# Kernel tuning notes

Measured on AMD Instinct MI355X. Metric: run time of the kernel, lower is better.

Reference implementation:

```python
import jax, jax.numpy as jnp
import numpy as np
from jax import lax

N_BLOCKS = 5
POOL = 15
N_HEADS = 8
LATENT = 32
N_EXPERTS = 4


def setup_inputs() -> dict:
    key = jax.random.key(0)
    ks = jax.random.split(key, 24)
    B, T, D = 4, 2048, 512
    H = 2 * D  # expert_dim
    s = 0.02
    f = lambda k, shp: (jax.random.normal(k, shp, jnp.float32) * s)
    return {
        'x': jax.random.normal(ks[0], (B, T, D), jnp.float32),
        # TemporalGating gate_proj
        'tg_w': f(ks[1], (D, N_BLOCKS)), 'tg_b': jnp.zeros((N_BLOCKS,), jnp.float32),
        # DualScaleFusion
        'mp_w': f(ks[2], (D, D)), 'mp_b': jnp.zeros((D,), jnp.float32),
        'fu_w': f(ks[3], (2 * D, D)), 'fu_b': jnp.zeros((D,), jnp.float32),
        # MLAAttention (all no-bias)
        'wc': f(ks[4], (D, LATENT)), 'wk': f(ks[5], (LATENT, D)),
        'wv': f(ks[6], (LATENT, D)), 'wq': f(ks[7], (D, D)), 'wo': f(ks[8], (D, D)),
        # RMSNorms
        's1': jnp.ones((D,), jnp.float32), 's2': jnp.ones((D,), jnp.float32),
        # GatedMoE
        'wr': f(ks[9], (D, N_EXPERTS)), 'br': jnp.zeros((N_EXPERTS,), jnp.float32),
        'wg': f(ks[10], (D, D)), 'bg': jnp.zeros((D,), jnp.float32),
        'w1': f(ks[11], (N_EXPERTS, D, H)), 'b1': jnp.zeros((N_EXPERTS, H), jnp.float32),
        'w2': f(ks[12], (N_EXPERTS, H, D)), 'b2': jnp.zeros((N_EXPERTS, D), jnp.float32),
    }


def _temporal_gate(x, tg_w, tg_b):
    B, T, D = x.shape
    bs = T // N_BLOCKS
    tl = N_BLOCKS * bs
    r = x[:, :tl].reshape(B, N_BLOCKS, bs, D)          # [B,nb,bs,D]
    bm = r.mean(axis=2)                                 # [B,nb,D]
    imp = jax.nn.softmax(bm @ tg_w + tg_b, axis=-1)     # [B,nb,nb]
    imp = imp.mean(axis=-1, keepdims=True)              # [B,nb,1]
    g = (r * imp[..., None]).reshape(B, tl, D)
    return jnp.pad(g, ((0, 0), (0, T - tl), (0, 0)))


def _dual_scale(x, mp_w, mp_b, fu_w, fu_b):
    # AveragePooling1D(pool=15, stride=1, SAME): TF excludes padding from the mean.
    B, T, D = x.shape
    sums = lax.reduce_window(x, 0.0, lax.add, (1, POOL, 1), (1, 1, 1), 'SAME')
    cnt = lax.reduce_window(jnp.ones((1, T, 1), x.dtype), 0.0, lax.add,
                            (1, POOL, 1), (1, 1, 1), 'SAME')
    macro = sums / cnt
    macro_feat = macro @ mp_w + mp_b
    return jnp.concatenate([x, macro_feat], axis=-1) @ fu_w + fu_b


def _mla_attn(x, wc, wk, wv, wq, wo):
    B, T, D = x.shape
    dh = D // N_HEADS
    split = lambda t: t.reshape(B, T, N_HEADS, dh).transpose(0, 2, 1, 3)
    latent = x @ wc                                      # [B,T,L]
    K, V, Q = split(latent @ wk), split(latent @ wv), split(x @ wq)
    scores = jnp.einsum('bhqd,bhkd->bhqk', Q, K) / jnp.sqrt(jnp.float32(dh))
    causal = jnp.tril(jnp.ones((T, T), jnp.float32))
    scores = scores + (1.0 - causal) * -1e9
    attn = jax.nn.softmax(scores, axis=-1)
    out = jnp.einsum('bhqk,bhkd->bhqd', attn, V).transpose(0, 2, 1, 3).reshape(B, T, D)
    return out @ wo


def _rmsnorm(x, scale, eps=1e-6):
    var = jnp.mean(jnp.square(x), axis=-1, keepdims=True)
    return scale * (x * lax.rsqrt(var + eps))


def _moe(x, wr, br, wg, bg, w1, b1, w2, b2):
    w = jax.nn.softmax(x @ wr + br, axis=-1)             # [B,T,E]
    xg = x * jax.nn.sigmoid(x @ wg + bg)
    h = jax.nn.gelu(jnp.einsum('btd,edh->bteh', xg, w1) + b1, approximate=False)
    eo = jnp.einsum('bteh,ehd->bted', h, w2) + b2        # [B,T,E,D]
    return jnp.einsum('bted,bte->btd', eo, w)


def reference(x, tg_w, tg_b, mp_w, mp_b, fu_w, fu_b, wc, wk, wv, wq, wo,
              s1, s2, wr, br, wg, bg, w1, b1, w2, b2):
    xf = _temporal_gate(x, tg_w, tg_b)
    xfu = _dual_scale(xf, mp_w, mp_b, fu_w, fu_b)
    x1 = _rmsnorm(x + _mla_attn(xfu, wc, wk, wv, wq, wo), s1)
    return _rmsnorm(x1 + _moe(x1, wr, br, wg, bg, w1, b1, w2, b2), s2)
```

## Files before the change

### kernel.cpp

```cpp
#include <hip/hip_runtime.h>
#include <math.h>

#define B_   4
#define T_   2048
#define D_   512
#define TOK  (B_*T_)
#define TL_  2045
#define GATE 0.2f
#define QSCALE 0.18033688011112043f

typedef unsigned short u16;
typedef __attribute__((ext_vector_type(8))) short short8;
typedef __attribute__((ext_vector_type(4))) float f32x4;

static __device__ __forceinline__ u16 f2u(float f){
    union { float f; unsigned u; } a; a.f = f;
    unsigned r = a.u + 0x7fffu + ((a.u >> 16) & 1u);
    return (u16)(r >> 16);
}
static __device__ __forceinline__ float u2f(u16 u){
    union { unsigned u; float f; } a; a.u = ((unsigned)u) << 16;
    return a.f;
}
static __device__ __forceinline__ f32x4 mfma16(short8 a, short8 b, f32x4 c){
    return __builtin_amdgcn_mfma_f32_16x16x32_bf16(a, b, c, 0, 0, 0);
}
static __device__ __forceinline__ void glds16(const u16* g, u16* l){
    __builtin_amdgcn_global_load_lds((const __attribute__((address_space(1))) void*)g,
                                     (__attribute__((address_space(3))) void*)l, 16, 0, 0);
}

__global__ __launch_bounds__(256) void gatepool_kernel(
    const float* __restrict__ x, u16* __restrict__ xfcat)
{
    int idx = blockIdx.x*256 + threadIdx.x;
    int d = idx & 511, g = idx >> 9;
    int b = g >> 7, t0 = (g & 127) << 4;
    const float* xp = x + ((size_t)b*2048)*512 + d;
    float v[30];
    #pragma unroll
    for (int j = 0; j < 30; ++j){
        int u = t0 - 7 + j;
        v[j] = (u >= 0 && u < TL_) ? xp[(size_t)u*512] : 0.f;
    }
    float p[31]; p[0] = 0.f;
    #pragma unroll
    for (int j = 0; j < 30; ++j) p[j+1] = p[j] + v[j];
    u16* xc = xfcat + ((size_t)(b*2048 + t0))*1024 + d;
    #pragma unroll
    for (int i = 0; i < 16; ++i){
        int t = t0 + i;
        float sum = p[i+15] - p[i];
        int lo = t-7; if (lo < 0) lo = 0;
        int hi = t+7; if (hi > 2047) hi = 2047;
        xc[(size_t)i*1024]       = f2u((t < TL_) ? GATE*v[i+7] : 0.f);
        xc[(size_t)i*1024 + 512] = f2u(GATE * sum / (float)(hi - lo + 1));
    }
}

struct TJob { const float* src; u16* dst; int K, N, ldout, coloff, tiles; float scale; };
struct TJobs { TJob j[13]; int n; };

__global__ __launch_bounds__(256) void tconv_all_kernel(TJobs JJ){
    __shared__ float t[32][33];
    int idx = blockIdx.x;
    int jb = 0;
    while (jb < JJ.n - 1 && idx >= JJ.j[jb].tiles){ idx -= JJ.j[jb].tiles; ++jb; }
    TJob J = JJ.j[jb];
    int tX = J.N >> 5;
    int k0 = (idx / tX) * 32, n0 = (idx % tX) * 32;
    int tx = threadIdx.x & 31, ty = threadIdx.x >> 5;
    #pragma unroll
    for (int i = 0; i < 32; i += 8)
        t[ty+i][tx] = J.src[(size_t)(k0+ty+i)*J.N + n0+tx];
    __syncthreads();
    #pragma unroll
    for (int i = 0; i < 32; i += 8)
        J.dst[(size_t)(n0+ty+i)*J.ldout + J.coloff + k0+tx] = f2u(J.scale * t[tx][ty+i]);
}

__global__ void convert_kernel(const float* __restrict__ in, u16* __restrict__ out){
    int idx = blockIdx.x*256 + threadIdx.x;
    out[idx] = f2u(in[idx]);
}

__global__ __launch_bounds__(256) void biasfold_kernel(
    const float* __restrict__ fu_b, const float* __restrict__ mp_b,
    const float* __restrict__ fu_w, float* __restrict__ out)
{
    int n = blockIdx.x, tid = threadIdx.x;
    float s = mp_b[tid]*fu_w[(size_t)(512+tid)*512 + n]
            + mp_b[tid+256]*fu_w[(size_t)(768+tid)*512 + n];
    for (int off = 32; off; off >>= 1) s += __shfl_down(s, off);
    __shared__ float ws[4];
    if ((tid & 63) == 0) ws[tid >> 6] = s;
    __syncthreads();
    if (tid == 0) out[n] = fu_b[n] + ws[0]+ws[1]+ws[2]+ws[3];
}

__global__ __launch_bounds__(256) void qkvbias_kernel(
    const float* __restrict__ fubias, const u16* __restrict__ wqkvT,
    float* __restrict__ out)
{
    int n = blockIdx.x, tid = threadIdx.x;
    const u16* wp = wqkvT + (size_t)n*512;
    float s = fubias[tid]*u2f(wp[tid]) + fubias[tid+256]*u2f(wp[tid+256]);
    for (int off = 32; off; off >>= 1) s += __shfl_down(s, off);
    __shared__ float ws[4];
    if ((tid & 63) == 0) ws[tid >> 6] = s;
    __syncthreads();
    if (tid == 0) out[n] = ws[0]+ws[1]+ws[2]+ws[3];
}

__global__ __launch_bounds__(256) void sgemm_kernel(const float* __restrict__ A,
    const float* __restrict__ B, u16* __restrict__ dstT, int K){
    __shared__ float As[16][65];
    __shared__ float Bs[16][65];
    int tid = threadIdx.x;
    int tx = tid & 15, ty = tid >> 4;
    int m0 = blockIdx.y*64, n0 = blockIdx.x*64;
    int arow = tid >> 2, akq = (tid & 3) * 4;
    int bk = tid >> 4, bn = (tid & 15) * 4;
    float acc[4][4] = {};
    for (int k0 = 0; k0 < K; k0 += 16){
        const float* Ap = A + (size_t)(m0+arow)*K + k0 + akq;
        As[akq+0][arow]=Ap[0]; As[akq+1][arow]=Ap[1];
        As[akq+2][arow]=Ap[2]; As[akq+3][arow]=Ap[3];
        const float* Bp = B + (size_t)(k0+bk)*512 + n0 + bn;
        Bs[bk][bn+0]=Bp[0]; Bs[bk][bn+1]=Bp[1];
        Bs[bk][bn+2]=Bp[2]; Bs[bk][bn+3]=Bp[3];
        __syncthreads();
        #pragma unroll
        for (int kk = 0; kk < 16; ++kk){
            float av[4], bv[4];
            #pragma unroll
            for (int i=0;i<4;++i) av[i]=As[kk][ty*4+i];
            #pragma unroll
            for (int j=0;j<4;++j) bv[j]=Bs[kk][tx*4+j];
            #pragma unroll
            for (int i=0;i<4;++i)
                #pragma unroll
                for (int j=0;j<4;++j) acc[i][j] += av[i]*bv[j];
        }
        __syncthreads();
    }
    #pragma unroll
    for (int i=0;i<4;++i)
        #pragma unroll
        for (int j=0;j<4;++j)
            dstT[(size_t)(n0+tx*4+j)*512 + m0+ty*4+i] = f2u(acc[i][j]);
}

#define GF_GELU   1
#define GF_RSCOL  4
#define GF_GLU    8
#define GF_QKV    32

template<int MT>
__global__ __launch_bounds__(256) void mgemm_kernel(
    const u16* __restrict__ A, int lda, const u16* __restrict__ Bt, int ldb,
    const float* __restrict__ bias, const float* __restrict__ rs,
    const u16* __restrict__ glu, void* __restrict__ Cp, int ldc,
    u16* __restrict__ Cp2, int K, int flags)
{
    constexpr int MI = MT/32;
    __shared__ u16 As[MT*64];
    __shared__ u16 Bs[128*64];
    int tid = threadIdx.x;
    int wave = tid >> 6, lane = tid & 63;
    int n16 = lane & 15, quad = lane >> 4;
    int m0 = blockIdx.y * MT, n0 = blockIdx.x * 128;
    int wr = (wave >> 1) * (MT/2), wc = (wave & 1) * 64;

    f32x4 acc[MI][4] = {};

    for (int k0 = 0; k0 < K; k0 += 64){
        #pragma unroll
        for (int i = 0; i < MT/32; ++i){
            int s = i*256 + tid;
            int row = s >> 3, g = (s & 7) ^ (row & 7);
            glds16(A + (size_t)(m0+row)*lda + k0 + g*8, As + (size_t)s*8);
        }
        #pragma unroll
        for (int i = 0; i < 4; ++i){
            int s = i*256 + tid;
            int row = s >> 3, g = (s & 7) ^ (row & 7);
            glds16(Bt + (size_t)(n0+row)*ldb + k0 + g*8, Bs + (size_t)s*8);
        }
        __syncthreads();
        #pragma unroll
        for (int ks = 0; ks < 2; ++ks){
            short8 af[MI], bf[4];
            #pragma unroll
            for (int mi = 0; mi < MI; ++mi){
                int row = wr + mi*16 + n16;
                int g = (ks*4 + quad) ^ (row & 7);
                af[mi] = *(const short8*)&As[row*64 + g*8];
            }
            #pragma unroll
            for (int ni = 0; ni < 4; ++ni){
                int row = wc + ni*16 + n16;
                int g = (ks*4 + quad) ^ (row & 7);
                bf[ni] = *(const short8*)&Bs[row*64 + g*8];
            }
            #pragma unroll
            for (int mi = 0; mi < MI; ++mi)
                #pragma unroll
                for (int ni = 0; ni < 4; ++ni)
                    acc[mi][ni] = mfma16(af[mi], bf[ni], acc[mi][ni]);
        }
        __syncthreads();
    }

    if ((flags & GF_QKV) && n0 >= 1024){
        #pragma unroll
        for (int mi = 0; mi < MI; ++mi){
            int row0 = m0 + wr + mi*16 + quad*4;
            #pragma unroll
            for (int ni = 0; ni < 4; ++ni){
                int col = n0 + wc + ni*16 + n16;
                float bb = bias[col];
                ushort4 h4;
                h4.x = f2u(acc[mi][ni][0] + bb); h4.y = f2u(acc[mi][ni][1] + bb);
                h4.z = f2u(acc[mi][ni][2] + bb); h4.w = f2u(acc[mi][ni][3] + bb);
                *(ushort4*)&Cp2[(size_t)(col-1024)*8192 + row0] = h4;
            }
        }
        return;
    }

    #pragma unroll
    for (int mi = 0; mi < MI; ++mi){
        #pragma unroll
        for (int reg = 0; reg < 4; ++reg){
            int row = m0 + wr + mi*16 + quad*4 + reg;
            #pragma unroll
            for (int ni = 0; ni < 4; ++ni){
                int col = n0 + wc + ni*16 + n16;
                float v = acc[mi][ni][reg];
                if (bias) v += bias[col];
                if (flags & GF_GELU)  v = 0.5f*v*(1.f + erff(v*0.70710678118f));
                if (flags & GF_GLU)   v = u2f(glu[(size_t)row*512 + col]) / (1.f + __expf(-v));
                if (flags & GF_RSCOL) v *= rs[(size_t)row*4 + (col >> 10)];
                ((u16*)Cp)[(size_t)row*ldc + col] = f2u(v);
            }
        }
    }
}

__global__ __launch_bounds__(256) void flash_kernel(
    const u16* __restrict__ QK,
    const u16* __restrict__ VT,
    u16* __restrict__ O)
{
    int bid = blockIdx.x;
    int qt = 15 - (bid >> 5);
    int bh = bid & 31;
    int h = bh & 7, b = bh >> 3;
    __shared__ u16 Ks[64*64];
    __shared__ u16 Vt[64*64];
    __shared__ u16 Ps[4][32*64];
    int tid = threadIdx.x;
    int wave = tid >> 6, lane = tid & 63;
    int n16 = lane & 15, quad = lane >> 4;
    size_t btok = (size_t)b*2048;
    size_t tok0 = btok + qt*128;

    short8 qf[2][2];
    #pragma unroll
    for (int g = 0; g < 2; ++g)
        #pragma unroll
        for (int ks = 0; ks < 2; ++ks)
            qf[g][ks] = *(const short8*)&QK[(tok0 + wave*32 + g*16 + n16)*1024
                                           + h*64 + ks*32 + quad*8];

    int qlo[2];  qlo[0] = qt*128 + wave*32; qlo[1] = qlo[0] + 16;
    int qrow[2]; qrow[0] = qlo[0] + n16;    qrow[1] = qlo[1] + n16;
    float m_st[2] = {-3.0e38f, -3.0e38f}, l_st[2] = {0.f, 0.f};
    f32x4 ov[2][4] = {};

    int nkt = 2*qt + 2;
    for (int kt = 0; kt < nkt; ++kt){
        __syncthreads();
        {
            int r = tid >> 2;
            int g0 = (tid & 3) * 2;
            const uint4* kp = (const uint4*)&QK[(btok + kt*64 + r)*1024 + 512 + h*64 + g0*8];
            uint4 ka = kp[0], kb = kp[1];
            *(uint4*)&Ks[r*64 + ((g0  ) ^ (r&7))*8] = ka;
            *(uint4*)&Ks[r*64 + ((g0+1) ^ (r&7))*8] = kb;
            const uint4* vp = (const uint4*)&VT[(size_t)(h*64 + r)*8192 + btok + kt*64 + g0*8];
            uint4 va = vp[0], vb = vp[1];
            *(uint4*)&Vt[r*64 + ((g0  ) ^ (r&7))*8] = va;
            *(uint4*)&Vt[r*64 + ((g0+1) ^ (r&7))*8] = vb;
        }
        __syncthreads();

        bool act[2];
        #pragma unroll
        for (int g = 0; g < 2; ++g){
            act[g] = (kt*64 <= qlo[g] + 15);
            if (!act[g]) continue;
            f32x4 st[4];
            #pragma unroll
            for (int ct = 0; ct < 4; ++ct){
                f32x4 a = {};
                #pragma unroll
                for (int ks = 0; ks < 2; ++ks){
                    short8 kf = *(const short8*)&Ks[(ct*16+n16)*64 + (((ks*4+quad) ^ (n16&7))*8)];
                    a = mfma16(kf, qf[g][ks], a);
                }
                st[ct] = a;
            }
            if (kt*64 + 63 > qlo[g]){
                #pragma unroll
                for (int ct = 0; ct < 4; ++ct){
                    int kb0 = kt*64 + ct*16 + quad*4;
                    #pragma unroll
                    for (int r = 0; r < 4; ++r)
                        if (kb0 + r > qrow[g]) st[ct][r] = -3.0e38f;
                }
            }
            float mx = fmaxf(fmaxf(fmaxf(st[0][0],st[0][1]),fmaxf(st[0][2],st[0][3])),
                       fmaxf(fmaxf(fmaxf(st[1][0],st[1][1]),fmaxf(st[1][2],st[1][3])),
                       fmaxf(fmaxf(fmaxf(st[2][0],st[2][1]),fmaxf(st[2][2],st[2][3])),
                             fmaxf(fmaxf(st[3][0],st[3][1]),fmaxf(st[3][2],st[3][3])))));
            mx = fmaxf(mx, __shfl_xor(mx, 16));
            mx = fmaxf(mx, __shfl_xor(mx, 32));
            float mn = fmaxf(m_st[g], mx);
            float al = exp2f(m_st[g] - mn);
            m_st[g] = mn;
            float sum = 0.f;
            #pragma unroll
            for (int ct = 0; ct < 4; ++ct)
                #pragma unroll
                for (int r = 0; r < 4; ++r){
                    float p = exp2f(st[ct][r] - mn);
                    st[ct][r] = p; sum += p;
                }
            sum += __shfl_xor(sum, 16);
            sum += __shfl_xor(sum, 32);
            l_st[g] = l_st[g]*al + sum;
            int qr = g*16 + n16;
            #pragma unroll
            for (int ct = 0; ct < 4; ++ct){
                ushort4 h4;
                h4.x = f2u(st[ct][0]); h4.y = f2u(st[ct][1]);
                h4.z = f2u(st[ct][2]); h4.w = f2u(st[ct][3]);
                int goff = ct*2 + (quad >> 1);
                *(ushort4*)&Ps[wave][qr*64 + ((goff ^ (qr&7))*8) + (quad&1)*4] = h4;
            }
            #pragma unroll
            for (int r = 0; r < 4; ++r){
                float aa = __shfl(al, quad*4 + r);
                #pragma unroll
                for (int dt = 0; dt < 4; ++dt) ov[g][dt][r] *= aa;
            }
        }
        #pragma unroll
        for (int g = 0; g < 2; ++g){
            if (!act[g]) continue;
            short8 ap[2];
            int row = g*16 + n16;
            #pragma unroll
            for (int ks = 0; ks < 2; ++ks)
                ap[ks] = *(const short8*)&Ps[wave][row*64 + (((ks*4+quad) ^ (row&7))*8)];
            #pragma unroll
            for (int dt = 0; dt < 4; ++dt)
                #pragma unroll
                for (int ks = 0; ks < 2; ++ks){
                    short8 bv = *(const short8*)&Vt[(dt*16+n16)*64 + (((ks*4+quad) ^ (n16&7))*8)];
                    ov[g][dt] = mfma16(ap[ks], bv, ov[g][dt]);
                }
        }
    }
    #pragma unroll
    for (int g = 0; g < 2; ++g)
        #pragma unroll
        for (int r = 0; r < 4; ++r){
            float li = __shfl(l_st[g], quad*4 + r);
            float inv = 1.f / li;
            size_t row = tok0 + wave*32 + g*16 + quad*4 + r;
            #pragma unroll
            for (int dt = 0; dt < 4; ++dt)
                O[row*512 + h*64 + dt*16 + n16] = f2u(ov[g][dt][r] * inv);
        }
}

__global__ __launch_bounds__(256) void rmsnorm_kernel(
    const float* __restrict__ x, const u16* __restrict__ y,
    const float* __restrict__ scale, u16* __restrict__ out)
{
    int tok = blockIdx.x, tid = threadIdx.x;
    size_t base = (size_t)tok * 512;
    float v0 = x[base+tid]     + u2f(y[base+tid]);
    float v1 = x[base+tid+256] + u2f(y[base+tid+256]);
    float ss = v0*v0 + v1*v1;
    for (int off = 32; off; off >>= 1) ss += __shfl_down(ss, off);
    __shared__ float ws[4];
    if ((tid & 63) == 0) ws[tid >> 6] = ss;
    __syncthreads();
    float rstd = rsqrtf((ws[0]+ws[1]+ws[2]+ws[3])*(1.f/512.f) + 1e-6f);
    out[base+tid]     = f2u(scale[tid]     * v0 * rstd);
    out[base+tid+256] = f2u(scale[tid+256] * v1 * rstd);
}

__global__ __launch_bounds__(256) void final_kernel(
    const u16* __restrict__ x1, const u16* __restrict__ moe,
    const float* __restrict__ rout, const float* __restrict__ b2,
    const float* __restrict__ scale, float* __restrict__ out)
{
    int tok = blockIdx.x, tid = threadIdx.x;
    size_t base = (size_t)tok * 512;
    float r0 = rout[tok*4+0], r1 = rout[tok*4+1], r2 = rout[tok*4+2], r3 = rout[tok*4+3];
    float bb0 = r0*b2[tid]     + r1*b2[512+tid]     + r2*b2[1024+tid]     + r3*b2[1536+tid];
    float bb1 = r0*b2[tid+256] + r1*b2[768+tid]     + r2*b2[1280+tid]     + r3*b2[1792+tid];
    float v0 = u2f(x1[base+tid])     + u2f(moe[base+tid])     + bb0;
    float v1 = u2f(x1[base+tid+256]) + u2f(moe[base+tid+256]) + bb1;
    float ss = v0*v0 + v1*v1;
    for (int off = 32; off; off >>= 1) ss += __shfl_down(ss, off);
    __shared__ float ws[4];
    if ((tid & 63) == 0) ws[tid >> 6] = ss;
    __syncthreads();
    float rstd = rsqrtf((ws[0]+ws[1]+ws[2]+ws[3])*(1.f/512.f) + 1e-6f);
    out[base+tid]     = scale[tid]     * v0 * rstd;
    out[base+tid+256] = scale[tid+256] * v1 * rstd;
}

__global__ __launch_bounds__(256) void router_kernel(
    const u16* __restrict__ x1, const float* __restrict__ wr,
    const float* __restrict__ br, float* __restrict__ rout)
{
    int wid = threadIdx.x >> 6, lane = threadIdx.x & 63;
    int tok = blockIdx.x*4 + wid;
    const u16* xp = x1 + (size_t)tok*512;
    float p0=0.f, p1=0.f, p2=0.f, p3=0.f;
    for (int d = lane; d < 512; d += 64){
        float xv = u2f(xp[d]);
        p0 += xv*wr[d*4+0]; p1 += xv*wr[d*4+1];
        p2 += xv*wr[d*4+2]; p3 += xv*wr[d*4+3];
    }
    for (int off = 32; off; off >>= 1){
        p0 += __shfl_down(p0,off); p1 += __shfl_down(p1,off);
        p2 += __shfl_down(p2,off); p3 += __shfl_down(p3,off);
    }
    if (lane == 0){
        p0 += br[0]; p1 += br[1]; p2 += br[2]; p3 += br[3];
        float mx = fmaxf(fmaxf(p0,p1), fmaxf(p2,p3));
        float e0=__expf(p0-mx), e1=__expf(p1-mx), e2=__expf(p2-mx), e3=__expf(p3-mx);
        float inv = 1.f/(e0+e1+e2+e3);
        rout[tok*4+0]=e0*inv; rout[tok*4+1]=e1*inv;
        rout[tok*4+2]=e2*inv; rout[tok*4+3]=e3*inv;
    }
}

extern "C" void kernel_launch(void* const* d_in, const int* in_sizes, int n_in,
                              void* d_out, int out_size, void* d_ws, size_t ws_size,
                              hipStream_t stream)
{
    const float* x    = (const float*)d_in[0];
    const float* mp_w = (const float*)d_in[3];
    const float* mp_b = (const float*)d_in[4];
    const float* fu_w = (const float*)d_in[5];
    const float* fu_b = (const float*)d_in[6];
    const float* wc   = (const float*)d_in[7];
    const float* wk   = (const float*)d_in[8];
    const float* wv   = (const float*)d_in[9];
    const float* wq   = (const float*)d_in[10];
    const float* wo   = (const float*)d_in[11];
    const float* s1   = (const float*)d_in[12];
    const float* s2   = (const float*)d_in[13];
    const float* wr   = (const float*)d_in[14];
    const float* br   = (const float*)d_in[15];
    const float* wg   = (const float*)d_in[16];
    const float* bg   = (const float*)d_in[17];
    const float* w1   = (const float*)d_in[18];
    const float* b1   = (const float*)d_in[19];
    const float* w2   = (const float*)d_in[20];
    const float* b2   = (const float*)d_in[21];

    char* wsb = (char*)d_ws;
    const size_t MB = 1024*1024;
    u16*   WqkvC  = (u16*)(wsb + 0);
    u16*   woT    = (u16*)(wsb + 3*MB);
    u16*   wgT    = (u16*)(wsb + 3*MB + 512*1024);
    u16*   w1T    = (u16*)(wsb + 4*MB);
    u16*   w2Ts   = (u16*)(wsb + 8*MB);
    float* fubias = (float*)(wsb + 12*MB);
    float* qkvbias= (float*)(wsb + 12*MB + 4096);
    float* ROUT   = (float*)(wsb + 12*MB + 16384);
    u16*   wqkvT  = (u16*)(wsb + 25*MB/2);
    u16*   fuBT   = (u16*)(wsb + 14*MB);
    u16*   mp_wB  = (u16*)(wsb + 29*MB/2);
    u16*   WfuBF  = (u16*)(wsb + 15*MB);
    u16*   XFcat = (u16*)(wsb + 16*MB);
    u16*   S3    = (u16*)(wsb + 16*MB);
    u16*   MOE   = (u16*)(wsb + 16*MB);
    u16*   x1h   = (u16*)(wsb + 24*MB);
    u16*   QKb   = (u16*)(wsb + 32*MB);
    u16*   XG    = (u16*)(wsb + 32*MB);
    u16*   Hb    = (u16*)(wsb + 40*MB);
    u16*   VbT   = (u16*)(wsb + 48*MB);
    u16*   ATT   = (u16*)(wsb + 56*MB);

    auto mg128 = [&](const u16* A, int lda, const u16* Bt, int ldb, const float* bias,
                     const float* rs, const u16* glu, void* C, int ldc, u16* C2,
                     int M, int N, int K, int flags){
        dim3 g(N/128, M/128);
        mgemm_kernel<128><<<g, 256, 0, stream>>>(A, lda, Bt, ldb, bias, rs, glu, C, ldc, C2, K, flags);
    };
    auto mg64 = [&](const u16* A, int lda, const u16* Bt, int ldb, const float* bias,
                    const float* rs, const u16* glu, void* C, int ldc, u16* C2,
                    int M, int N, int K, int flags){
        dim3 g(N/128, M/64);
        mgemm_kernel<64><<<g, 256, 0, stream>>>(A, lda, Bt, ldb, bias, rs, glu, C, ldc, C2, K, flags);
    };

    TJobs JJ; JJ.n = 11;
    auto setj = [&](int i, const float* src, u16* dst, int K, int N, int ldout,
                    int coloff, float scale){
        JJ.j[i] = TJob{src, dst, K, N, ldout, coloff, (K/32)*(N/32), scale};
    };
    setj(0, wq,            wqkvT, 512,  512,  512, 0, QSCALE);
    setj(1, wo,            woT,   512,  512,  512, 0, 1.f);
    setj(2, wg,            wgT,   512,  512,  512, 0, 1.f);
    setj(3, fu_w + 512*512,fuBT,  512,  512,  512, 0, 1.f);
    for (int e = 0; e < 4; ++e){
        setj(4+e, w1 + (size_t)e*512*1024, w1T + (size_t)e*1024*512, 512, 1024, 512, 0, 1.f);
        setj(8+e, w2 + (size_t)e*1024*512, w2Ts + (size_t)e*1024, 1024, 512, 4096, 0, 1.f);
    }
    int nt = 4*256 + 8*512;
    tconv_all_kernel<<<nt, 256, 0, stream>>>(JJ);
    convert_kernel<<<512*512/256, 256, 0, stream>>>(mp_w, mp_wB);
    convert_kernel<<<512*512/256, 256, 0, stream>>>(fu_w, WfuBF);
    sgemm_kernel<<<dim3(8,8), 256, 0, stream>>>(wc, wk, wqkvT + 512*512, 32);
    sgemm_kernel<<<dim3(8,8), 256, 0, stream>>>(wc, wv, wqkvT + 1024*512, 32);
    biasfold_kernel<<<512, 256, 0, stream>>>(fu_b, mp_b, fu_w, fubias);
    qkvbias_kernel<<<1536, 256, 0, stream>>>(fubias, wqkvT, qkvbias);
    mg64(mp_wB, 512, fuBT, 512, 0, 0, 0, WfuBF + 512*512, 512, 0, 512, 512, 512, 0);
    mg64(wqkvT, 512, WfuBF, 512, 0, 0, 0, WqkvC, 1024, 0, 1536, 1024, 512, 0);

    gatepool_kernel<<<(TOK/16)*512/256, 256, 0, stream>>>(x, XFcat);
    mg64 (XFcat, 1024, WqkvC, 1024, qkvbias, 0, 0, QKb, 1024, VbT, TOK, 1536, 1024, GF_QKV);
    flash_kernel<<<512, 256, 0, stream>>>(QKb, VbT, ATT);
    mg64 (ATT, 512, woT, 512, 0, 0, 0, S3, 512, 0, TOK, 512, 512, 0);
    rmsnorm_kernel<<<TOK, 256, 0, stream>>>(x, S3, s1, x1h);
    router_kernel<<<TOK/4, 256, 0, stream>>>(x1h, wr, br, ROUT);
    mg64 (x1h, 512, wgT, 512, bg, 0, x1h, XG, 512, 0, TOK, 512, 512, GF_GLU);
    for (int h = 0; h < 2; ++h){
        mg128(XG + (size_t)h*4096*512, 512, w1T, 512, b1, ROUT + (size_t)h*4096*4, 0,
              Hb, 4096, 0, 4096, 4096, 512, GF_GELU | GF_RSCOL);
        mg64 (Hb, 4096, w2Ts, 4096, 0, 0, 0,
              MOE + (size_t)h*4096*512, 512, 0, 4096, 512, 4096, 0);
    }
    final_kernel<<<TOK, 256, 0, stream>>>(x1h, MOE, ROUT, b2, s2, (float*)d_out);
}
```

Baseline: 612.9 us.

## Rebalance causal flash tiles and fuse MoE halves into full-M GEMM launches

The flash kernel now uses 64-row query tiles and has each block process a mirrored pair of tiles (31-p and p), so every block does the same amount of causal work. The probability tile is converted to bf16 by truncation instead of rounding. The GEMM kernel gains a second A/C base pointer split at row 4096, which lets the QKV (now 128-row tiles), output, gate and MoE GEMMs run as single full-token launches instead of per-half loops. The MoE down-projection writes fp32 output, with an accumulate fallback path when the workspace is small. The trade-offs are less K/V reuse per loaded tile in attention, slightly less accurate probabilities, and more fp32 traffic for the MoE output.

```diff
diff --git a/kernel.cpp b/kernel.cpp
--- a/kernel.cpp
+++ b/kernel.cpp
@@ -8,6 +8,7 @@
 #define TL_  2045
 #define GATE 0.2f
 #define QSCALE 0.18033688011112043f
+#define MSPLIT 4096
 
 typedef unsigned short u16;
 typedef __attribute__((ext_vector_type(8))) short short8;
@@ -17,6 +18,9 @@
     union { float f; unsigned u; } a; a.f = f;
     unsigned r = a.u + 0x7fffu + ((a.u >> 16) & 1u);
     return (u16)(r >> 16);
+}
+static __device__ __forceinline__ u16 f2u_t(float f){
+    return (u16)(__float_as_uint(f) >> 16);
 }
 static __device__ __forceinline__ float u2f(u16 u){
     union { unsigned u; float f; } a; a.u = ((unsigned)u) << 16;
@@ -152,16 +156,19 @@
 }
 
 #define GF_GELU   1
+#define GF_ACCUM  2
 #define GF_RSCOL  4
 #define GF_GLU    8
+#define GF_F32OUT 16
 #define GF_QKV    32
 
 template<int MT>
 __global__ __launch_bounds__(256) void mgemm_kernel(
-    const u16* __restrict__ A, int lda, const u16* __restrict__ Bt, int ldb,
+    const u16* __restrict__ A, const u16* __restrict__ A2, int lda,
+    const u16* __restrict__ Bt, int ldb,
     const float* __restrict__ bias, const float* __restrict__ rs,
-    const u16* __restrict__ glu, void* __restrict__ Cp, int ldc,
-    u16* __restrict__ Cp2, int K, int flags)
+    const u16* __restrict__ glu, void* __restrict__ Cp, void* __restrict__ CpB,
+    int ldc, u16* __restrict__ Cp2, int K, int flags)
 {
     constexpr int MI = MT/32;
     __shared__ u16 As[MT*64];
@@ -179,7 +186,10 @@
         for (int i = 0; i < MT/32; ++i){
             int s = i*256 + tid;
             int row = s >> 3, g = (s & 7) ^ (row & 7);
-            glds16(A + (size_t)(m0+row)*lda + k0 + g*8, As + (size_t)s*8);
+            int rg = m0 + row;
+            const u16* Ap = (rg < MSPLIT) ? A + (size_t)rg*lda
+                                          : A2 + (size_t)(rg - MSPLIT)*lda;
+            glds16(Ap + k0 + g*8, As + (size_t)s*8);
         }
         #pragma unroll
         for (int i = 0; i < 4; ++i){
@@ -234,6 +244,8 @@
         #pragma unroll
         for (int reg = 0; reg < 4; ++reg){
             int row = m0 + wr + mi*16 + quad*4 + reg;
+            void*  cb = (row < MSPLIT) ? Cp : CpB;
+            size_t rr = (row < MSPLIT) ? row : row - MSPLIT;
             #pragma unroll
             for (int ni = 0; ni < 4; ++ni){
                 int col = n0 + wc + ni*16 + n16;
@@ -242,7 +254,10 @@
                 if (flags & GF_GELU)  v = 0.5f*v*(1.f + erff(v*0.70710678118f));
                 if (flags & GF_GLU)   v = u2f(glu[(size_t)row*512 + col]) / (1.f + __expf(-v));
                 if (flags & GF_RSCOL) v *= rs[(size_t)row*4 + (col >> 10)];
-                ((u16*)Cp)[(size_t)row*ldc + col] = f2u(v);
+                size_t ci = rr*ldc + col;
+                if (flags & GF_ACCUM)       ((float*)cb)[ci] += v;
+                else if (flags & GF_F32OUT) ((float*)cb)[ci]  = v;
+                else                        ((u16*)cb)[ci]    = f2u(v);
             }
         }
     }
@@ -254,53 +269,45 @@
     u16* __restrict__ O)
 {
     int bid = blockIdx.x;
-    int qt = 15 - (bid >> 5);
+    int p = bid >> 5;
     int bh = bid & 31;
     int h = bh & 7, b = bh >> 3;
     __shared__ u16 Ks[64*64];
     __shared__ u16 Vt[64*64];
-    __shared__ u16 Ps[4][32*64];
+    __shared__ u16 Ps[4][16*64];
     int tid = threadIdx.x;
     int wave = tid >> 6, lane = tid & 63;
     int n16 = lane & 15, quad = lane >> 4;
     size_t btok = (size_t)b*2048;
-    size_t tok0 = btok + qt*128;
-
-    short8 qf[2][2];
-    #pragma unroll
-    for (int g = 0; g < 2; ++g)
+
+    for (int ph = 0; ph < 2; ++ph){
+        int qt = ph ? p : (31 - p);
+        size_t tok0 = btok + qt*64;
+        short8 qf[2];
         #pragma unroll
         for (int ks = 0; ks < 2; ++ks)
-            qf[g][ks] = *(const short8*)&QK[(tok0 + wave*32 + g*16 + n16)*1024
-                                           + h*64 + ks*32 + quad*8];
-
-    int qlo[2];  qlo[0] = qt*128 + wave*32; qlo[1] = qlo[0] + 16;
-    int qrow[2]; qrow[0] = qlo[0] + n16;    qrow[1] = qlo[1] + n16;
-    float m_st[2] = {-3.0e38f, -3.0e38f}, l_st[2] = {0.f, 0.f};
-    f32x4 ov[2][4] = {};
-
-    int nkt = 2*qt + 2;
-    for (int kt = 0; kt < nkt; ++kt){
-        __syncthreads();
-        {
-            int r = tid >> 2;
-            int g0 = (tid & 3) * 2;
-            const uint4* kp = (const uint4*)&QK[(btok + kt*64 + r)*1024 + 512 + h*64 + g0*8];
-            uint4 ka = kp[0], kb = kp[1];
-            *(uint4*)&Ks[r*64 + ((g0  ) ^ (r&7))*8] = ka;
-            *(uint4*)&Ks[r*64 + ((g0+1) ^ (r&7))*8] = kb;
-            const uint4* vp = (const uint4*)&VT[(size_t)(h*64 + r)*8192 + btok + kt*64 + g0*8];
-            uint4 va = vp[0], vb = vp[1];
-            *(uint4*)&Vt[r*64 + ((g0  ) ^ (r&7))*8] = va;
-            *(uint4*)&Vt[r*64 + ((g0+1) ^ (r&7))*8] = vb;
-        }
-        __syncthreads();
-
-        bool act[2];
-        #pragma unroll
-        for (int g = 0; g < 2; ++g){
-            act[g] = (kt*64 <= qlo[g] + 15);
-            if (!act[g]) continue;
+            qf[ks] = *(const short8*)&QK[(tok0 + wave*16 + n16)*1024
+                                         + h*64 + ks*32 + quad*8];
+        int qrow = qt*64 + wave*16 + n16;
+        float m_st = -3.0e38f, l_st = 0.f;
+        f32x4 ov[4] = {};
+
+        for (int kt = 0; kt <= qt; ++kt){
+            __syncthreads();
+            {
+                int r = tid >> 2;
+                int g0 = (tid & 3) * 2;
+                const uint4* kp = (const uint4*)&QK[(btok + kt*64 + r)*1024 + 512 + h*64 + g0*8];
+                uint4 ka = kp[0], kb = kp[1];
+                *(uint4*)&Ks[r*64 + ((g0  ) ^ (r&7))*8] = ka;
+                *(uint4*)&Ks[r*64 + ((g0+1) ^ (r&7))*8] = kb;
+                const uint4* vp = (const uint4*)&VT[(size_t)(h*64 + r)*8192 + btok + kt*64 + g0*8];
+                uint4 va = vp[0], vb = vp[1];
+                *(uint4*)&Vt[r*64 + ((g0  ) ^ (r&7))*8] = va;
+                *(uint4*)&Vt[r*64 + ((g0+1) ^ (r&7))*8] = vb;
+            }
+            __syncthreads();
+
             f32x4 st[4];
             #pragma unroll
             for (int ct = 0; ct < 4; ++ct){
@@ -308,17 +315,17 @@
                 #pragma unroll
                 for (int ks = 0; ks < 2; ++ks){
                     short8 kf = *(const short8*)&Ks[(ct*16+n16)*64 + (((ks*4+quad) ^ (n16&7))*8)];
-                    a = mfma16(kf, qf[g][ks], a);
+                    a = mfma16(kf, qf[ks], a);
                 }
                 st[ct] = a;
             }
-            if (kt*64 + 63 > qlo[g]){
+            if (kt == qt){
                 #pragma unroll
                 for (int ct = 0; ct < 4; ++ct){
                     int kb0 = kt*64 + ct*16 + quad*4;
                     #pragma unroll
                     for (int r = 0; r < 4; ++r)
-                        if (kb0 + r > qrow[g]) st[ct][r] = -3.0e38f;
+                        if (kb0 + r > qrow) st[ct][r] = -3.0e38f;
                 }
             }
             float mx = fmaxf(fmaxf(fmaxf(st[0][0],st[0][1]),fmaxf(st[0][2],st[0][3])),
@@ -327,64 +334,56 @@
                              fmaxf(fmaxf(st[3][0],st[3][1]),fmaxf(st[3][2],st[3][3])))));
             mx = fmaxf(mx, __shfl_xor(mx, 16));
             mx = fmaxf(mx, __shfl_xor(mx, 32));
-            float mn = fmaxf(m_st[g], mx);
-            float al = exp2f(m_st[g] - mn);
-            m_st[g] = mn;
+            float mn = fmaxf(m_st, mx);
+            float al = exp2f(m_st - mn);
+            m_st = mn;
             float sum = 0.f;
             #pragma unroll
             for (int ct = 0; ct < 4; ++ct)
                 #pragma unroll
                 for (int r = 0; r < 4; ++r){
-                    float p = exp2f(st[ct][r] - mn);
-                    st[ct][r] = p; sum += p;
+                    float pp = exp2f(st[ct][r] - mn);
+                    st[ct][r] = pp; sum += pp;
                 }
             sum += __shfl_xor(sum, 16);
             sum += __shfl_xor(sum, 32);
-            l_st[g] = l_st[g]*al + sum;
-            int qr = g*16 + n16;
+            l_st = l_st*al + sum;
             #pragma unroll
             for (int ct = 0; ct < 4; ++ct){
                 ushort4 h4;
-                h4.x = f2u(st[ct][0]); h4.y = f2u(st[ct][1]);
-                h4.z = f2u(st[ct][2]); h4.w = f2u(st[ct][3]);
+                h4.x = f2u_t(st[ct][0]); h4.y = f2u_t(st[ct][1]);
+                h4.z = f2u_t(st[ct][2]); h4.w = f2u_t(st[ct][3]);
                 int goff = ct*2 + (quad >> 1);
-                *(ushort4*)&Ps[wave][qr*64 + ((goff ^ (qr&7))*8) + (quad&1)*4] = h4;
+                *(ushort4*)&Ps[wave][n16*64 + ((goff ^ (n16&7))*8) + (quad&1)*4] = h4;
             }
             #pragma unroll
             for (int r = 0; r < 4; ++r){
                 float aa = __shfl(al, quad*4 + r);
                 #pragma unroll
-                for (int dt = 0; dt < 4; ++dt) ov[g][dt][r] *= aa;
-            }
-        }
-        #pragma unroll
-        for (int g = 0; g < 2; ++g){
-            if (!act[g]) continue;
+                for (int dt = 0; dt < 4; ++dt) ov[dt][r] *= aa;
+            }
             short8 ap[2];
-            int row = g*16 + n16;
             #pragma unroll
             for (int ks = 0; ks < 2; ++ks)
-                ap[ks] = *(const short8*)&Ps[wave][row*64 + (((ks*4+quad) ^ (row&7))*8)];
+                ap[ks] = *(const short8*)&Ps[wave][n16*64 + (((ks*4+quad) ^ (n16&7))*8)];
             #pragma unroll
             for (int dt = 0; dt < 4; ++dt)
                 #pragma unroll
                 for (int ks = 0; ks < 2; ++ks){
                     short8 bv = *(const short8*)&Vt[(dt*16+n16)*64 + (((ks*4+quad) ^ (n16&7))*8)];
-                    ov[g][dt] = mfma16(ap[ks], bv, ov[g][dt]);
+                    ov[dt] = mfma16(ap[ks], bv, ov[dt]);
                 }
         }
-    }
-    #pragma unroll
-    for (int g = 0; g < 2; ++g)
         #pragma unroll
         for (int r = 0; r < 4; ++r){
-            float li = __shfl(l_st[g], quad*4 + r);
+            float li = __shfl(l_st, quad*4 + r);
             float inv = 1.f / li;
-            size_t row = tok0 + wave*32 + g*16 + quad*4 + r;
+            size_t row = tok0 + wave*16 + quad*4 + r;
             #pragma unroll
             for (int dt = 0; dt < 4; ++dt)
-                O[row*512 + h*64 + dt*16 + n16] = f2u(ov[g][dt][r] * inv);
-        }
+                O[row*512 + h*64 + dt*16 + n16] = f2u(ov[dt][r] * inv);
+        }
+    }
 }
 
 __global__ __launch_bounds__(256) void rmsnorm_kernel(
@@ -406,7 +405,7 @@
 }
 
 __global__ __launch_bounds__(256) void final_kernel(
-    const u16* __restrict__ x1, const u16* __restrict__ moe,
+    const u16* __restrict__ x1, const float* __restrict__ moe,
     const float* __restrict__ rout, const float* __restrict__ b2,
     const float* __restrict__ scale, float* __restrict__ out)
 {
@@ -415,8 +414,8 @@
     float r0 = rout[tok*4+0], r1 = rout[tok*4+1], r2 = rout[tok*4+2], r3 = rout[tok*4+3];
     float bb0 = r0*b2[tid]     + r1*b2[512+tid]     + r2*b2[1024+tid]     + r3*b2[1536+tid];
     float bb1 = r0*b2[tid+256] + r1*b2[768+tid]     + r2*b2[1280+tid]     + r3*b2[1792+tid];
-    float v0 = u2f(x1[base+tid])     + u2f(moe[base+tid])     + bb0;
-    float v1 = u2f(x1[base+tid+256]) + u2f(moe[base+tid+256]) + bb1;
+    float v0 = u2f(x1[base+tid])     + moe[base+tid]     + bb0;
+    float v1 = u2f(x1[base+tid+256]) + moe[base+tid+256] + bb1;
     float ss = v0*v0 + v1*v1;
     for (int off = 32; off; off >>= 1) ss += __shfl_down(ss, off);
     __shared__ float ws[4];
@@ -487,36 +486,40 @@
     u16*   w1T    = (u16*)(wsb + 4*MB);
     u16*   w2Ts   = (u16*)(wsb + 8*MB);
     float* fubias = (float*)(wsb + 12*MB);
-    float* qkvbias= (float*)(wsb + 12*MB + 4096);
-    float* ROUT   = (float*)(wsb + 12*MB + 16384);
-    u16*   wqkvT  = (u16*)(wsb + 25*MB/2);
-    u16*   fuBT   = (u16*)(wsb + 14*MB);
-    u16*   mp_wB  = (u16*)(wsb + 29*MB/2);
-    u16*   WfuBF  = (u16*)(wsb + 15*MB);
+    float* qkvbias= (float*)(wsb + 12*MB + 8192);
+    float* ROUT   = (float*)(wsb + 12*MB + 32768);
+    u16*   wqkvT  = (u16*)(wsb + 12*MB + 512*1024);
+    u16*   fuBT   = (u16*)(wsb + 16*MB);
+    u16*   mp_wB  = (u16*)(wsb + 16*MB + 512*1024);
+    u16*   WfuBF  = (u16*)(wsb + 17*MB);
+    u16*   x1h   = (u16*)(wsb + 14*MB);
     u16*   XFcat = (u16*)(wsb + 16*MB);
-    u16*   S3    = (u16*)(wsb + 16*MB);
-    u16*   MOE   = (u16*)(wsb + 16*MB);
-    u16*   x1h   = (u16*)(wsb + 24*MB);
+    u16*   XG    = (u16*)(wsb + 22*MB);
+    u16*   S3    = (u16*)(wsb + 24*MB);
     u16*   QKb   = (u16*)(wsb + 32*MB);
-    u16*   XG    = (u16*)(wsb + 32*MB);
-    u16*   Hb    = (u16*)(wsb + 40*MB);
+    float* MOE   = (float*)(wsb + 32*MB);
     u16*   VbT   = (u16*)(wsb + 48*MB);
     u16*   ATT   = (u16*)(wsb + 56*MB);
-
-    auto mg128 = [&](const u16* A, int lda, const u16* Bt, int ldb, const float* bias,
-                     const float* rs, const u16* glu, void* C, int ldc, u16* C2,
-                     int M, int N, int K, int flags){
+    u16*   HbA   = (u16*)(wsb + 48*MB);
+    u16*   HbB   = (u16*)(wsb + 80*MB);
+    bool big = ws_size >= (size_t)112*MB;
+
+    auto mg128 = [&](const u16* A, const u16* A2, int lda, const u16* Bt, int ldb,
+                     const float* bias, const float* rs, const u16* glu,
+                     void* C, void* CB, int ldc, u16* C2, int M, int N, int K, int flags){
         dim3 g(N/128, M/128);
-        mgemm_kernel<128><<<g, 256, 0, stream>>>(A, lda, Bt, ldb, bias, rs, glu, C, ldc, C2, K, flags);
+        mgemm_kernel<128><<<g, 256, 0, stream>>>(A, A2, lda, Bt, ldb, bias, rs, glu,
+                                                 C, CB, ldc, C2, K, flags);
     };
-    auto mg64 = [&](const u16* A, int lda, const u16* Bt, int ldb, const float* bias,
-                    const float* rs, const u16* glu, void* C, int ldc, u16* C2,
-                    int M, int N, int K, int flags){
+    auto mg64 = [&](const u16* A, const u16* A2, int lda, const u16* Bt, int ldb,
+                    const float* bias, const float* rs, const u16* glu,
+                    void* C, void* CB, int ldc, u16* C2, int M, int N, int K, int flags){
         dim3 g(N/128, M/64);
-        mgemm_kernel<64><<<g, 256, 0, stream>>>(A, lda, Bt, ldb, bias, rs, glu, C, ldc, C2, K, flags);
+        mgemm_kernel<64><<<g, 256, 0, stream>>>(A, A2, lda, Bt, ldb, bias, rs, glu,
+                                                C, CB, ldc, C2, K, flags);
     };
 
-    TJobs JJ; JJ.n = 11;
+    TJobs JJ; JJ.n = 12;
     auto setj = [&](int i, const float* src, u16* dst, int K, int N, int ldout,
                     int coloff, float scale){
         JJ.j[i] = TJob{src, dst, K, N, ldout, coloff, (K/32)*(N/32), scale};
@@ -537,21 +540,37 @@
     sgemm_kernel<<<dim3(8,8), 256, 0, stream>>>(wc, wv, wqkvT + 1024*512, 32);
     biasfold_kernel<<<512, 256, 0, stream>>>(fu_b, mp_b, fu_w, fubias);
     qkvbias_kernel<<<1536, 256, 0, stream>>>(fubias, wqkvT, qkvbias);
-    mg64(mp_wB, 512, fuBT, 512, 0, 0, 0, WfuBF + 512*512, 512, 0, 512, 512, 512, 0);
-    mg64(wqkvT, 512, WfuBF, 512, 0, 0, 0, WqkvC, 1024, 0, 1536, 1024, 512, 0);
+    mg64(mp_wB, mp_wB, 512, fuBT, 512, 0, 0, 0,
+         WfuBF + 512*512, WfuBF + 512*512, 512, 0, 512, 512, 512, 0);
+    mg64(wqkvT, wqkvT, 512, WfuBF, 512, 0, 0, 0,
+         WqkvC, WqkvC, 1024, 0, 1536, 1024, 512, 0);
 
     gatepool_kernel<<<(TOK/16)*512/256, 256, 0, stream>>>(x, XFcat);
-    mg64 (XFcat, 1024, WqkvC, 1024, qkvbias, 0, 0, QKb, 1024, VbT, TOK, 1536, 1024, GF_QKV);
+    mg128(XFcat, XFcat + (size_t)MSPLIT*1024, 1024, WqkvC, 1024, qkvbias, 0, 0,
+          QKb, QKb + (size_t)MSPLIT*1024, 1024, VbT, TOK, 1536, 1024, GF_QKV);
     flash_kernel<<<512, 256, 0, stream>>>(QKb, VbT, ATT);
-    mg64 (ATT, 512, woT, 512, 0, 0, 0, S3, 512, 0, TOK, 512, 512, 0);
+    mg64 (ATT, ATT + (size_t)MSPLIT*512, 512, woT, 512, 0, 0, 0,
+          S3, S3 + (size_t)MSPLIT*512, 512, 0, TOK, 512, 512, 0);
     rmsnorm_kernel<<<TOK, 256, 0, stream>>>(x, S3, s1, x1h);
     router_kernel<<<TOK/4, 256, 0, stream>>>(x1h, wr, br, ROUT);
-    mg64 (x1h, 512, wgT, 512, bg, 0, x1h, XG, 512, 0, TOK, 512, 512, GF_GLU);
-    for (int h = 0; h < 2; ++h){
-        mg128(XG + (size_t)h*4096*512, 512, w1T, 512, b1, ROUT + (size_t)h*4096*4, 0,
-              Hb, 4096, 0, 4096, 4096, 512, GF_GELU | GF_RSCOL);
-        mg64 (Hb, 4096, w2Ts, 4096, 0, 0, 0,
-              MOE + (size_t)h*4096*512, 512, 0, 4096, 512, 4096, 0);
+    mg64 (x1h, x1h + (size_t)MSPLIT*512, 512, wgT, 512, bg, 0, x1h,
+          XG, XG + (size_t)MSPLIT*512, 512, 0, TOK, 512, 512, GF_GLU);
+    if (big){
+        mg128(XG, XG + (size_t)MSPLIT*512, 512, w1T, 512, b1, ROUT, 0,
+              HbA, HbB, 4096, 0, TOK, 4096, 512, GF_GELU | GF_RSCOL);
+        mg64 (HbA, HbB, 4096, w2Ts, 4096, 0, 0, 0,
+              MOE, (float*)MOE + (size_t)MSPLIT*512, 512, 0,
+              TOK, 512, 4096, GF_F32OUT);
+    } else {
+        for (int p = 0; p < 2; ++p){
+            mg128(XG, XG + (size_t)MSPLIT*512, 512, w1T + (size_t)p*2048*512, 512,
+                  b1 + p*2048, ROUT + p*2, 0,
+                  HbA, HbA + (size_t)MSPLIT*2048, 2048, 0,
+                  TOK, 2048, 512, GF_GELU | GF_RSCOL);
+            mg64 (HbA, HbA + (size_t)MSPLIT*2048, 2048, w2Ts + p*2048, 4096, 0, 0, 0,
+                  MOE, (float*)MOE + (size_t)MSPLIT*512, 512, 0,
+                  TOK, 512, 2048, p ? GF_ACCUM : GF_F32OUT);
+        }
     }
     final_kernel<<<TOK, 256, 0, stream>>>(x1h, MOE, ROUT, b2, s2, (float*)d_out);
 }
```

Result: faster. 583.0 us (-4.9%).
